# Optimization experiments

Hardware: AMD Instinct MI355X
Metric: run time of the kernel (lower is better)

Reference implementation:

```python
import jax, jax.numpy as jnp
import numpy as np

N9, N10, F = 6000, 9000, 128
ALPHA = 0.2  # LeakyReLU negative slope
NEG_INF = -9e15


def setup_inputs() -> dict:
    key = jax.random.key(0)
    k1, k2, k3, k4, k5 = jax.random.split(key, 5)
    U_9 = jax.random.normal(k1, (N9, F), dtype=jnp.float32) * 0.03
    U_10 = jax.random.normal(k2, (N10, F), dtype=jnp.float32) * 0.03
    # xavier_uniform with gain=1.414 for a: limit = gain*sqrt(6/(fan_in+fan_out))
    lim = 1.414 * np.sqrt(6.0 / (2 * F + 1))
    a = jax.random.uniform(k3, (2 * F, 1), dtype=jnp.float32, minval=-lim, maxval=lim)
    # sparse 0/1 code-mapping adjacencies, avg degree ~4
    adj_9to10 = (jax.random.uniform(k4, (N9, N10)) < 4.0 / N10).astype(jnp.float32)
    adj_10to9 = (jax.random.uniform(k5, (N10, N9)) < 4.0 / N9).astype(jnp.float32)
    return {"version": 0, "U_9": U_9, "U_10": U_10, "a": a,
            "adj_9to10": adj_9to10, "adj_10to9": adj_10to9}


def _gat(query, key_feat, adj, a):
    # a splits into the query-half and key-half of the attention vector
    Fd = query.shape[1]
    a1 = a[:Fd, 0]   # [F]
    a2 = a[Fd:, 0]   # [F]
    qa1 = query @ a1        # [Nq]
    qa2 = query @ a2        # [Nq]
    ka2 = key_feat @ a2     # [Nk]
    # self column: leakyrelu([q, q] @ a)
    self_e = jax.nn.leaky_relu(qa1 + qa2, ALPHA)                 # [Nq]
    # cross scores at edge positions: leakyrelu(q_i.a1 + k_j.a2);
    # non-edge entries differ from the torch sparse->dense zeros but are
    # masked to -9e15 below, so the output math is identical.
    e_cross = jax.nn.leaky_relu(qa1[:, None] + ka2[None, :], ALPHA)  # [Nq, Nk]
    ones_col = jnp.ones((query.shape[0], 1), dtype=adj.dtype)
    adj_full = jnp.concatenate([ones_col, adj], axis=1)          # [Nq, Nk+1]
    scores = jnp.concatenate([self_e[:, None], e_cross], axis=1)  # [Nq, Nk+1]
    scores = jnp.where(adj_full > 0, scores, NEG_INF)
    attn = jax.nn.softmax(scores, axis=-1) * adj_full
    attn = jnp.where(jnp.isnan(attn), 0.0, attn)
    h_prime = attn[:, :1] * query + attn[:, 1:] @ key_feat       # [Nq, F]
    return jax.nn.elu(h_prime)


def reference(version, U_9, U_10, a, adj_9to10, adj_10to9):
    if version == 0:  # 'mimiciv_icd9'
        return _gat(U_9, U_10, adj_9to10, a)
    else:
        return _gat(U_10, U_9, adj_10to9, a)
```

## Files before the change

kernel.cpp:

```cpp
#include <hip/hip_runtime.h>
#include <math.h>

#define N9     6000
#define N10    9000
#define FDIM   128
#define ALPHA  0.2f
#define MAXNBR 64
#define ROWBLOCKS 2048

typedef float f32x4 __attribute__((ext_vector_type(4)));

__global__ __launch_bounds__(256)
void gat_fused_kernel(const int* __restrict__ version,
                      const float* __restrict__ U9,
                      const float* __restrict__ U10,
                      const float* __restrict__ a,
                      const float* __restrict__ adj9to10,
                      const float* __restrict__ adj10to9,
                      float* __restrict__ out) {
    const int v  = version[0];
    const int nq = v ? N10 : N9;
    const int nk = v ? N9  : N10;
    const float* __restrict__ Q      = v ? U10 : U9;
    const float* __restrict__ K      = v ? U9  : U10;
    const float* __restrict__ adjmat = v ? adj10to9 : adj9to10;

    __shared__ float s_a1[FDIM];
    __shared__ float s_a2[FDIM];
    __shared__ float s_q[FDIM];
    __shared__ float s_k[MAXNBR][FDIM];
    __shared__ int   s_j[MAXNBR];
    __shared__ float s_e[MAXNBR];
    __shared__ float s_w[MAXNBR];
    __shared__ int   s_cnt;
    __shared__ float s_qa1, s_qa2, s_wself;

    const int t    = threadIdx.x;
    const int wave = t >> 6;
    const int lane = t & 63;

    if (t < FDIM) { s_a1[t] = a[t]; s_a2[t] = a[FDIM + t]; }
    __syncthreads();

    const int n4 = nk >> 2;

    for (int i = blockIdx.x; i < nq; i += gridDim.x) {
        if (t == 0) s_cnt = 0;
        __syncthreads();

        if (wave == 0) {
            const float* x = Q + (size_t)i * FDIM;
            float x0 = x[lane], x1 = x[lane + 64];
            s_q[lane] = x0; s_q[lane + 64] = x1;
            float s1 = x0 * s_a1[lane] + x1 * s_a1[lane + 64];
            float s2 = x0 * s_a2[lane] + x1 * s_a2[lane + 64];
            #pragma unroll
            for (int o = 32; o > 0; o >>= 1) {
                s1 += __shfl_down(s1, o);
                s2 += __shfl_down(s2, o);
            }
            if (lane == 0) { s_qa1 = s1; s_qa2 = s2; }
        }

        const f32x4* __restrict__ adj4 = (const f32x4*)(adjmat + (size_t)i * nk);
        for (int p0 = t; p0 < n4; p0 += 256 * 4) {
            const int p1 = p0 + 256, p2 = p0 + 512, p3 = p0 + 768;
            f32x4 r0 = __builtin_nontemporal_load(&adj4[p0]);
            f32x4 r1 = (f32x4)(0.f);
            f32x4 r2 = r1, r3 = r1;
            if (p1 < n4) r1 = __builtin_nontemporal_load(&adj4[p1]);
            if (p2 < n4) r2 = __builtin_nontemporal_load(&adj4[p2]);
            if (p3 < n4) r3 = __builtin_nontemporal_load(&adj4[p3]);

            f32x4 rr[4] = {r0, r1, r2, r3};
            int   pp[4] = {p0, p1, p2, p3};
            #pragma unroll
            for (int u = 0; u < 4; ++u) {
                f32x4 vv = rr[u];
                if (vv.x > 0.f || vv.y > 0.f || vv.z > 0.f || vv.w > 0.f) {
                    float va[4] = {vv.x, vv.y, vv.z, vv.w};
                    #pragma unroll
                    for (int c = 0; c < 4; ++c) {
                        if (va[c] > 0.f) {
                            int idx = atomicAdd(&s_cnt, 1);
                            if (idx < MAXNBR) s_j[idx] = pp[u] * 4 + c;
                        }
                    }
                }
            }
        }
        __syncthreads();

        const int cnt = (s_cnt < MAXNBR) ? s_cnt : MAXNBR;

        for (int c = wave; c < cnt; c += 4) {
            const int j = s_j[c];
            const float* k = K + (size_t)j * FDIM;
            float x0 = k[lane], x1 = k[lane + 64];
            s_k[c][lane] = x0; s_k[c][lane + 64] = x1;
            float s2 = x0 * s_a2[lane] + x1 * s_a2[lane + 64];
            #pragma unroll
            for (int o = 32; o > 0; o >>= 1) s2 += __shfl_down(s2, o);
            if (lane == 0) {
                float e = s_qa1 + s2;
                s_e[c] = (e >= 0.f) ? e : ALPHA * e;
            }
        }
        __syncthreads();

        if (t == 0) {
            float se = s_qa1 + s_qa2;
            se = (se >= 0.f) ? se : ALPHA * se;
            float m = se;
            for (int c = 0; c < cnt; ++c) m = fmaxf(m, s_e[c]);
            float wself = expf(se - m);
            float wsum  = wself;
            for (int c = 0; c < cnt; ++c) {
                float w = expf(s_e[c] - m);
                s_w[c] = w;
                wsum += w;
            }
            float inv = 1.f / wsum;
            s_wself = wself * inv;
            for (int c = 0; c < cnt; ++c) s_w[c] *= inv;
        }
        __syncthreads();

        if (t < FDIM) {
            float h = s_wself * s_q[t];
            for (int c = 0; c < cnt; ++c) h += s_w[c] * s_k[c][t];
            h = (h > 0.f) ? h : expm1f(h);
            out[(size_t)i * FDIM + t] = h;
        }
        __syncthreads();
    }
}

extern "C" void kernel_launch(void* const* d_in, const int* in_sizes, int n_in,
                              void* d_out, int out_size, void* d_ws, size_t ws_size,
                              hipStream_t stream) {
    const int*   d_version = (const int*)d_in[0];
    const float* d_U9      = (const float*)d_in[1];
    const float* d_U10     = (const float*)d_in[2];
    const float* d_a       = (const float*)d_in[3];
    const float* d_adj9    = (const float*)d_in[4];
    const float* d_adj10   = (const float*)d_in[5];
    float*       d_o       = (float*)d_out;

    gat_fused_kernel<<<ROWBLOCKS, 256, 0, stream>>>(
        d_version, d_U9, d_U10, d_a, d_adj9, d_adj10, d_o);
}
```

Measured before the change: 51.03 us.

## Assign one wavefront per query row and remove block-level barriers

Restructures the GAT kernel so each 64-lane wavefront handles a whole query row: it scans the adjacency row, gathers neighbours, runs the softmax and does the weighted sum. The block-wide syncthreads and single-thread softmax go away, and the grid grows to cover all rows with no grid-stride. Neighbour feature rows are now read from global memory twice instead of being staged in shared memory. Adjacency loads also drop the nontemporal hint, and the exponentials switch to the fast __expf intrinsic. Each row's adjacency scan now uses 64 lanes instead of 256, which means fewer loads in flight per row.

New measurement: 45.72 us. 10.4% less time.

```diff
diff --git a/kernel.cpp b/kernel.cpp
--- a/kernel.cpp
+++ b/kernel.cpp
@@ -6,18 +6,25 @@
 #define FDIM   128
 #define ALPHA  0.2f
 #define MAXNBR 64
-#define ROWBLOCKS 2048
+#define WPB    4
+#define GRID   ((N10 + WPB - 1) / WPB)
 
 typedef float f32x4 __attribute__((ext_vector_type(4)));
 
+__device__ __forceinline__ float wave_bcast_sum(float x) {
+    #pragma unroll
+    for (int o = 32; o > 0; o >>= 1) x += __shfl_xor(x, o);
+    return x;
+}
+
 __global__ __launch_bounds__(256)
-void gat_fused_kernel(const int* __restrict__ version,
-                      const float* __restrict__ U9,
-                      const float* __restrict__ U10,
-                      const float* __restrict__ a,
-                      const float* __restrict__ adj9to10,
-                      const float* __restrict__ adj10to9,
-                      float* __restrict__ out) {
+void gat_wave_kernel(const int* __restrict__ version,
+                     const float* __restrict__ U9,
+                     const float* __restrict__ U10,
+                     const float* __restrict__ a,
+                     const float* __restrict__ adj9to10,
+                     const float* __restrict__ adj10to9,
+                     float* __restrict__ out) {
     const int v  = version[0];
     const int nq = v ? N10 : N9;
     const int nk = v ? N9  : N10;
@@ -25,15 +32,10 @@
     const float* __restrict__ K      = v ? U9  : U10;
     const float* __restrict__ adjmat = v ? adj10to9 : adj9to10;
 
-    __shared__ float s_a1[FDIM];
-    __shared__ float s_a2[FDIM];
-    __shared__ float s_q[FDIM];
-    __shared__ float s_k[MAXNBR][FDIM];
-    __shared__ int   s_j[MAXNBR];
-    __shared__ float s_e[MAXNBR];
-    __shared__ float s_w[MAXNBR];
-    __shared__ int   s_cnt;
-    __shared__ float s_qa1, s_qa2, s_wself;
+    __shared__ float s_a1[FDIM], s_a2[FDIM];
+    __shared__ int   s_j[WPB][MAXNBR];
+    __shared__ float s_e[WPB][MAXNBR];
+    __shared__ int   s_cnt[WPB];
 
     const int t    = threadIdx.x;
     const int wave = t >> 6;
@@ -42,35 +44,30 @@
     if (t < FDIM) { s_a1[t] = a[t]; s_a2[t] = a[FDIM + t]; }
     __syncthreads();
 
+    const float a1lo = s_a1[lane], a1hi = s_a1[lane + 64];
+    const float a2lo = s_a2[lane], a2hi = s_a2[lane + 64];
+
+    const int gw = blockIdx.x * WPB + wave;
+    const int nw = gridDim.x * WPB;
     const int n4 = nk >> 2;
 
-    for (int i = blockIdx.x; i < nq; i += gridDim.x) {
-        if (t == 0) s_cnt = 0;
-        __syncthreads();
+    for (int i = gw; i < nq; i += nw) {
+        if (lane == 0) s_cnt[wave] = 0;
 
-        if (wave == 0) {
-            const float* x = Q + (size_t)i * FDIM;
-            float x0 = x[lane], x1 = x[lane + 64];
-            s_q[lane] = x0; s_q[lane + 64] = x1;
-            float s1 = x0 * s_a1[lane] + x1 * s_a1[lane + 64];
-            float s2 = x0 * s_a2[lane] + x1 * s_a2[lane + 64];
-            #pragma unroll
-            for (int o = 32; o > 0; o >>= 1) {
-                s1 += __shfl_down(s1, o);
-                s2 += __shfl_down(s2, o);
-            }
-            if (lane == 0) { s_qa1 = s1; s_qa2 = s2; }
-        }
+        const float* qr = Q + (size_t)i * FDIM;
+        float qx0 = qr[lane], qx1 = qr[lane + 64];
+        float qa1 = wave_bcast_sum(qx0 * a1lo + qx1 * a1hi);
+        float qa2 = wave_bcast_sum(qx0 * a2lo + qx1 * a2hi);
 
         const f32x4* __restrict__ adj4 = (const f32x4*)(adjmat + (size_t)i * nk);
-        for (int p0 = t; p0 < n4; p0 += 256 * 4) {
-            const int p1 = p0 + 256, p2 = p0 + 512, p3 = p0 + 768;
-            f32x4 r0 = __builtin_nontemporal_load(&adj4[p0]);
-            f32x4 r1 = (f32x4)(0.f);
-            f32x4 r2 = r1, r3 = r1;
-            if (p1 < n4) r1 = __builtin_nontemporal_load(&adj4[p1]);
-            if (p2 < n4) r2 = __builtin_nontemporal_load(&adj4[p2]);
-            if (p3 < n4) r3 = __builtin_nontemporal_load(&adj4[p3]);
+        int mycnt = 0;
+        for (int p0 = lane; p0 < n4; p0 += 64 * 4) {
+            const int p1 = p0 + 64, p2 = p0 + 128, p3 = p0 + 192;
+            f32x4 r0 = adj4[p0];
+            f32x4 r1 = (f32x4)(0.f), r2 = (f32x4)(0.f), r3 = (f32x4)(0.f);
+            if (p1 < n4) r1 = adj4[p1];
+            if (p2 < n4) r2 = adj4[p2];
+            if (p3 < n4) r3 = adj4[p3];
 
             f32x4 rr[4] = {r0, r1, r2, r3};
             int   pp[4] = {p0, p1, p2, p3};
@@ -82,57 +79,51 @@
                     #pragma unroll
                     for (int c = 0; c < 4; ++c) {
                         if (va[c] > 0.f) {
-                            int idx = atomicAdd(&s_cnt, 1);
-                            if (idx < MAXNBR) s_j[idx] = pp[u] * 4 + c;
+                            int idx = atomicAdd(&s_cnt[wave], 1);
+                            if (idx < MAXNBR) s_j[wave][idx] = pp[u] * 4 + c;
+                            ++mycnt;
                         }
                     }
                 }
             }
         }
-        __syncthreads();
+        int cnt = mycnt;
+        #pragma unroll
+        for (int o = 32; o > 0; o >>= 1) cnt += __shfl_xor(cnt, o);
+        if (cnt > MAXNBR) cnt = MAXNBR;
+        __threadfence_block();
 
-        const int cnt = (s_cnt < MAXNBR) ? s_cnt : MAXNBR;
+        for (int c = 0; c < cnt; ++c) {
+            const int j = s_j[wave][c];
+            const float* kr = K + (size_t)j * FDIM;
+            float d = wave_bcast_sum(kr[lane] * a2lo + kr[lane + 64] * a2hi);
+            float e = qa1 + d;
+            if (lane == 0) s_e[wave][c] = (e >= 0.f) ? e : ALPHA * e;
+        }
+        __threadfence_block();
 
-        for (int c = wave; c < cnt; c += 4) {
-            const int j = s_j[c];
-            const float* k = K + (size_t)j * FDIM;
-            float x0 = k[lane], x1 = k[lane + 64];
-            s_k[c][lane] = x0; s_k[c][lane + 64] = x1;
-            float s2 = x0 * s_a2[lane] + x1 * s_a2[lane + 64];
-            #pragma unroll
-            for (int o = 32; o > 0; o >>= 1) s2 += __shfl_down(s2, o);
-            if (lane == 0) {
-                float e = s_qa1 + s2;
-                s_e[c] = (e >= 0.f) ? e : ALPHA * e;
-            }
+        float se = qa1 + qa2;
+        se = (se >= 0.f) ? se : ALPHA * se;
+        float m = se;
+        for (int c = 0; c < cnt; ++c) m = fmaxf(m, s_e[wave][c]);
+        float wself = __expf(se - m);
+        float wsum  = wself;
+        for (int c = 0; c < cnt; ++c) wsum += __expf(s_e[wave][c] - m);
+        const float inv = 1.f / wsum;
+
+        float h0 = wself * inv * qx0;
+        float h1 = wself * inv * qx1;
+        for (int c = 0; c < cnt; ++c) {
+            const int j = s_j[wave][c];
+            const float w = __expf(s_e[wave][c] - m) * inv;
+            const float* kr = K + (size_t)j * FDIM;
+            h0 += w * kr[lane];
+            h1 += w * kr[lane + 64];
         }
-        __syncthreads();
-
-        if (t == 0) {
-            float se = s_qa1 + s_qa2;
-            se = (se >= 0.f) ? se : ALPHA * se;
-            float m = se;
-            for (int c = 0; c < cnt; ++c) m = fmaxf(m, s_e[c]);
-            float wself = expf(se - m);
-            float wsum  = wself;
-            for (int c = 0; c < cnt; ++c) {
-                float w = expf(s_e[c] - m);
-                s_w[c] = w;
-                wsum += w;
-            }
-            float inv = 1.f / wsum;
-            s_wself = wself * inv;
-            for (int c = 0; c < cnt; ++c) s_w[c] *= inv;
-        }
-        __syncthreads();
-
-        if (t < FDIM) {
-            float h = s_wself * s_q[t];
-            for (int c = 0; c < cnt; ++c) h += s_w[c] * s_k[c][t];
-            h = (h > 0.f) ? h : expm1f(h);
-            out[(size_t)i * FDIM + t] = h;
-        }
-        __syncthreads();
+        h0 = (h0 > 0.f) ? h0 : expm1f(h0);
+        h1 = (h1 > 0.f) ? h1 : expm1f(h1);
+        out[(size_t)i * FDIM + lane]      = h0;
+        out[(size_t)i * FDIM + lane + 64] = h1;
     }
 }
 
@@ -147,6 +138,6 @@
     const float* d_adj10   = (const float*)d_in[5];
     float*       d_o       = (float*)d_out;
 
-    gat_fused_kernel<<<ROWBLOCKS, 256, 0, stream>>>(
+    gat_wave_kernel<<<GRID, 256, 0, stream>>>(
         d_version, d_U9, d_U10, d_a, d_adj9, d_adj10, d_o);
 }
```
